# Performance work log

Measured on AMD Instinct MI355X. Metric: run time of the kernel, lower is better.

Reference implementation:

```python
import jax, jax.numpy as jnp
import numpy as np

EPS = 1e-12  # torch F.normalize eps
K = 32       # num_clusters (hardcoded in module)

def l2norm(v, axis):
    n = jnp.sqrt(jnp.sum(v * v, axis=axis, keepdims=True))
    return v / jnp.maximum(n, EPS)

def setup_inputs() -> dict:
    key = jax.random.key(0)
    k1, k2, k3, k4 = jax.random.split(key, 4)
    B, M, D = 64, 128, 2048
    x = jax.random.normal(k1, (B, M, D), dtype=jnp.float32)
    # ragged lengths in [1, M]
    lengths = jax.random.randint(k2, (B,), 0, M, dtype=jnp.int32) + 1
    init_sc = 1.0 / np.sqrt(D)
    W = init_sc * jax.random.normal(k3, (K, D), dtype=jnp.float32)  # fc1.weight
    C = init_sc * jax.random.normal(k4, (K, D), dtype=jnp.float32)  # centroids
    return {"x": x, "lengths": lengths, "W": W, "C": C}

def reference(x, lengths, W, C):
    # x: [B,M,D] padded frames, lengths: [B] valid frame counts
    B, M, D = x.shape
    mask = (jnp.arange(M)[None, :] < lengths[:, None]).astype(x.dtype)  # [B,M]
    cnt = lengths.astype(x.dtype)[:, None]                              # [B,1]
    # avg pooling over valid (raw, un-normalized) frames
    avgpool = jnp.sum(x * mask[:, :, None], axis=1) / cnt               # [B,D]
    # per-frame L2 normalize
    xn = l2norm(x, axis=-1)                                             # [B,M,D]
    # soft assignment: linear (no bias) + softmax over clusters
    logits = jnp.einsum('bmd,kd->bmk', xn, W)
    a = jax.nn.softmax(logits, axis=-1) * mask[:, :, None]              # [B,M,K]
    # VLAD residual aggregation, GEMM form:
    # sum_m a[b,m,k]*(xn[b,m,:] - C[k,:]) = (a^T xn) - C * sum_m a
    ax = jnp.einsum('bmk,bmd->bkd', a, xn)                              # [B,K,D]
    asum = jnp.sum(a, axis=1)                                           # [B,K]
    vlad = ax - asum[:, :, None] * C[None, :, :]                        # [B,K,D]
    # intra-normalize per cluster, flatten, global L2 normalize
    vlad = l2norm(vlad, axis=2)
    vlad = vlad.reshape(B, K * D)
    vlad = l2norm(vlad, axis=1)
    return jnp.concatenate([avgpool, vlad], axis=1)                     # [B, D + K*D]
```

## Files before the change

### kernel.cpp

```cpp
#include <hip/hip_runtime.h>
#include <math.h>

#define BB 64
#define MM 128
#define DDIM 2048
#define KK 32
#define NFR (BB*MM)
#define OUTROW (DDIM + KK*DDIM)

typedef __attribute__((ext_vector_type(8))) short bf16x8;
typedef __attribute__((ext_vector_type(4))) float f32x4;

__device__ __forceinline__ short f2bf(float f) {
  unsigned u = __builtin_bit_cast(unsigned, f);
  u += 0x7fffu + ((u >> 16) & 1u);
  return (short)(u >> 16);
}
__device__ __forceinline__ unsigned pack2(float lo, float hi) {
  return (unsigned)(unsigned short)f2bf(lo) | ((unsigned)(unsigned short)f2bf(hi) << 16);
}

__global__ __launch_bounds__(256) void k_prep(const float* __restrict__ W,
                                              short* __restrict__ Wb) {
  int i = (blockIdx.x * 256 + threadIdx.x) * 8;
  float4 a = *(const float4*)(W + i);
  float4 b = *(const float4*)(W + i + 4);
  bf16x8 o = {f2bf(a.x), f2bf(a.y), f2bf(a.z), f2bf(a.w),
              f2bf(b.x), f2bf(b.y), f2bf(b.z), f2bf(b.w)};
  *(bf16x8*)(Wb + i) = o;
}

__global__ __launch_bounds__(256, 2) void k_logits(const float* __restrict__ x,
    const int* __restrict__ lengths, const short* __restrict__ Wb,
    short* __restrict__ aT, float* __restrict__ asum_p) {
  const int t = threadIdx.x, wv = t >> 6, lane = t & 63;
  const int l15 = lane & 15, quad = lane >> 4;
  const int fg = blockIdx.x;
  const int g0 = fg * 16;
  const int b  = fg >> 3;
  const int m0 = (fg & 7) * 16;
  const int len = lengths[b];
  const bool av = (m0 + l15) < len;

  const float* xrow = x + (size_t)(g0 + l15) * DDIM + wv * 512 + quad * 8;
  const short* w0   = Wb + l15 * DDIM + wv * 512 + quad * 8;
  const short* w1   = w0 + 16 * DDIM;

  f32x4 c0 = {0.f, 0.f, 0.f, 0.f}, c1 = {0.f, 0.f, 0.f, 0.f};
  float ssq = 0.f;
  #pragma unroll
  for (int h = 0; h < 2; ++h) {
    float4 xa[8], xc[8];
    bf16x8 B0[8], B1[8];
    #pragma unroll
    for (int s = 0; s < 8; ++s) {
      const int so = h * 8 + s;
      if (av) {
        xa[s] = *(const float4*)(xrow + so * 32);
        xc[s] = *(const float4*)(xrow + so * 32 + 4);
      } else {
        xa[s] = make_float4(0.f, 0.f, 0.f, 0.f);
        xc[s] = make_float4(0.f, 0.f, 0.f, 0.f);
      }
      B0[s] = *(const bf16x8*)(w0 + so * 32);
      B1[s] = *(const bf16x8*)(w1 + so * 32);
    }
    #pragma unroll
    for (int s = 0; s < 8; ++s) {
      ssq = fmaf(xa[s].x, xa[s].x, ssq); ssq = fmaf(xa[s].y, xa[s].y, ssq);
      ssq = fmaf(xa[s].z, xa[s].z, ssq); ssq = fmaf(xa[s].w, xa[s].w, ssq);
      ssq = fmaf(xc[s].x, xc[s].x, ssq); ssq = fmaf(xc[s].y, xc[s].y, ssq);
      ssq = fmaf(xc[s].z, xc[s].z, ssq); ssq = fmaf(xc[s].w, xc[s].w, ssq);
      bf16x8 A = {f2bf(xa[s].x), f2bf(xa[s].y), f2bf(xa[s].z), f2bf(xa[s].w),
                  f2bf(xc[s].x), f2bf(xc[s].y), f2bf(xc[s].z), f2bf(xc[s].w)};
      c0 = __builtin_amdgcn_mfma_f32_16x16x32_bf16(A, B0[s], c0, 0, 0, 0);
      c1 = __builtin_amdgcn_mfma_f32_16x16x32_bf16(A, B1[s], c1, 0, 0, 0);
    }
  }

  ssq += __shfl_xor(ssq, 16, 64);
  ssq += __shfl_xor(ssq, 32, 64);
  __shared__ float sq[4][16];
  __shared__ float lg[4][16][33];
  if (quad == 0) sq[wv][l15] = ssq;
  #pragma unroll
  for (int r = 0; r < 4; ++r) {
    lg[wv][quad * 4 + r][l15]      = c0[r];
    lg[wv][quad * 4 + r][16 + l15] = c1[r];
  }
  __syncthreads();

  const int fr = t >> 4, kk = (t & 15) * 2;
  float s0 = 0.f, s1 = 0.f;
  #pragma unroll
  for (int w = 0; w < 4; ++w) { s0 += lg[w][fr][kk]; s1 += lg[w][fr][kk + 1]; }
  float ss  = sq[0][fr] + sq[1][fr] + sq[2][fr] + sq[3][fr];
  float inv = 1.f / fmaxf(sqrtf(ss), 1e-12f);
  s0 *= inv; s1 *= inv;
  float mx = fmaxf(s0, s1);
  mx = fmaxf(mx, __shfl_xor(mx, 1, 64));
  mx = fmaxf(mx, __shfl_xor(mx, 2, 64));
  mx = fmaxf(mx, __shfl_xor(mx, 4, 64));
  mx = fmaxf(mx, __shfl_xor(mx, 8, 64));
  float e0 = __expf(s0 - mx), e1 = __expf(s1 - mx);
  float se = e0 + e1;
  se += __shfl_xor(se, 1, 64);
  se += __shfl_xor(se, 2, 64);
  se += __shfl_xor(se, 4, 64);
  se += __shfl_xor(se, 8, 64);
  const bool valid = (m0 + fr) < len;
  float rr = valid ? (1.f / se) : 0.f;
  float a0 = e0 * rr, a1 = e1 * rr;

  __syncthreads();
  lg[0][fr][kk] = a0; lg[0][fr][kk + 1] = a1;
  __syncthreads();
  if (t < KK) {
    float s = 0.f;
    #pragma unroll
    for (int f = 0; f < 16; ++f) s += lg[0][f][t];
    asum_p[(size_t)fg * KK + t] = s;
  }
  short* ap = aT + (size_t)b * KK * MM + m0 + fr;
  ap[(size_t)kk * MM]       = f2bf(a0 * inv);
  ap[(size_t)(kk + 1) * MM] = f2bf(a1 * inv);
}

__global__ __launch_bounds__(256, 3) void k_vlad(const float* __restrict__ x,
    const int* __restrict__ lengths, const float* __restrict__ Cc,
    const short* __restrict__ aT, const float* __restrict__ asum_p,
    float* __restrict__ out, float* __restrict__ ssq_part) {
  const int t = threadIdx.x, wv = t >> 6, lane = t & 63;
  const int l15 = lane & 15, quad = lane >> 4;
  const int dc = blockIdx.x, b = blockIdx.y;
  const int dw0 = dc * 256 + wv * 64;
  const int len = lengths[b];

  __shared__ short xbt[4][64][40];
  __shared__ float vst[16][268];
  __shared__ float asl[KK];
  __shared__ float ss32[KK];

  if (t < KK) {
    float s = 0.f;
    #pragma unroll
    for (int p = 0; p < 8; ++p) s += asum_p[(size_t)(b * 8 + p) * KK + t];
    asl[t] = s;
  }

  const float* xb  = x  + (size_t)b * MM * DDIM;
  const short* at0 = aT + (size_t)b * KK * MM + (size_t)l15 * MM + quad * 8;

  const int q4   = l15 * 4;
  const int mrow = quad * 2;
  const int keyw = l15 & 3;
  const int keyr = (l15 >> 2) & 3;

  bf16x8 A0[4], A1[4];
  #pragma unroll
  for (int ms = 0; ms < 4; ++ms) {
    A0[ms] = *(const bf16x8*)(at0 + ms * 32);
    A1[ms] = *(const bf16x8*)(at0 + 16 * MM + ms * 32);
  }

  f32x4 acc[2][4];
  #pragma unroll
  for (int kt = 0; kt < 2; ++kt)
    #pragma unroll
    for (int nt = 0; nt < 4; ++nt) acc[kt][nt] = (f32x4){0.f, 0.f, 0.f, 0.f};
  float avg[4] = {0.f, 0.f, 0.f, 0.f};

  #pragma unroll
  for (int ms = 0; ms < 4; ++ms) {
    float4 v0[4], v1[4];
    #pragma unroll
    for (int p = 0; p < 4; ++p) {
      const int m = ms * 32 + p * 8 + mrow;
      const float* xr = xb + (size_t)m * DDIM + dw0 + q4;
      v0[p] = (m < len) ? *(const float4*)xr : make_float4(0.f, 0.f, 0.f, 0.f);
      v1[p] = (m + 1 < len) ? *(const float4*)(xr + DDIM)
                            : make_float4(0.f, 0.f, 0.f, 0.f);
    }
    #pragma unroll
    for (int p = 0; p < 4; ++p) {
      avg[0] += v0[p].x + v1[p].x;
      avg[1] += v0[p].y + v1[p].y;
      avg[2] += v0[p].z + v1[p].z;
      avg[3] += v0[p].w + v1[p].w;
      const int mls = (p ^ keyw) * 8 + mrow;
      *(unsigned*)&xbt[wv][q4 + 0][mls] = pack2(v0[p].x, v1[p].x);
      *(unsigned*)&xbt[wv][q4 + 1][mls] = pack2(v0[p].y, v1[p].y);
      *(unsigned*)&xbt[wv][q4 + 2][mls] = pack2(v0[p].z, v1[p].z);
      *(unsigned*)&xbt[wv][q4 + 3][mls] = pack2(v0[p].w, v1[p].w);
    }
    #pragma unroll
    for (int nt = 0; nt < 4; ++nt) {
      bf16x8 B = *(const bf16x8*)&xbt[wv][nt * 16 + l15][(quad ^ keyr) * 8];
      acc[0][nt] = __builtin_amdgcn_mfma_f32_16x16x32_bf16(A0[ms], B, acc[0][nt], 0, 0, 0);
      acc[1][nt] = __builtin_amdgcn_mfma_f32_16x16x32_bf16(A1[ms], B, acc[1][nt], 0, 0, 0);
    }
  }

  #pragma unroll
  for (int c = 0; c < 4; ++c) {
    avg[c] += __shfl_xor(avg[c], 16, 64);
    avg[c] += __shfl_xor(avg[c], 32, 64);
  }
  if (quad == 0) {
    float rl = 1.f / (float)len;
    *(float4*)(out + (size_t)b * OUTROW + dw0 + q4) =
        make_float4(avg[0] * rl, avg[1] * rl, avg[2] * rl, avg[3] * rl);
  }

  __syncthreads();
  float* orow = out + (size_t)b * OUTROW + DDIM;
  #pragma unroll
  for (int kt = 0; kt < 2; ++kt) {
    #pragma unroll
    for (int r = 0; r < 4; ++r) {
      const int kl = quad * 4 + r;
      const int k  = kt * 16 + kl;
      const float as = asl[k];
      #pragma unroll
      for (int nt = 0; nt < 4; ++nt) {
        const int d = dw0 + nt * 16 + l15;
        vst[kl][wv * 64 + nt * 16 + l15] =
            acc[kt][nt][r] - as * Cc[(size_t)k * DDIM + d];
      }
    }
    __syncthreads();
    #pragma unroll
    for (int it = 0; it < 4; ++it) {
      const int kl = it * 4 + wv;
      const int k  = kt * 16 + kl;
      float4 v = *(const float4*)&vst[kl][lane * 4];
      *(float4*)(orow + (size_t)k * DDIM + dc * 256 + lane * 4) = v;
      float sqv = fmaf(v.x, v.x, fmaf(v.y, v.y, fmaf(v.z, v.z, v.w * v.w)));
      sqv += __shfl_xor(sqv, 1, 64);
      sqv += __shfl_xor(sqv, 2, 64);
      sqv += __shfl_xor(sqv, 4, 64);
      sqv += __shfl_xor(sqv, 8, 64);
      sqv += __shfl_xor(sqv, 16, 64);
      sqv += __shfl_xor(sqv, 32, 64);
      if (lane == 0) ss32[k] = sqv;
    }
    __syncthreads();
  }
  if (t < KK)
    ssq_part[((size_t)dc * BB + b) * KK + t] = ss32[t];
}

__global__ __launch_bounds__(256) void k_norm(const float* __restrict__ ssq_part,
    float* __restrict__ out) {
  const int t = threadIdx.x;
  const int k = blockIdx.x;
  const int b = blockIdx.y;
  __shared__ float ssk[32];
  if (t < 32) {
    float sk = 0.f;
    #pragma unroll
    for (int dc = 0; dc < 8; ++dc)
      sk += ssq_part[((size_t)dc * BB + b) * KK + t];
    ssk[t] = sk;
  }
  __syncthreads();
  float gss = 0.f, iv_own = 0.f;
  #pragma unroll
  for (int kk = 0; kk < 32; ++kk) {
    float nk = sqrtf(ssk[kk]);
    float iv = 1.f / fmaxf(nk, 1e-12f);
    float nn = nk * iv;
    gss += nn * nn;
    if (kk == k) iv_own = iv;
  }
  float sc = iv_own / fmaxf(sqrtf(gss), 1e-12f);
  float* row = out + (size_t)b * OUTROW + DDIM + (size_t)k * DDIM;
  #pragma unroll
  for (int h = 0; h < 2; ++h) {
    float4* p = (float4*)(row + h * 1024 + t * 4);
    float4 v = *p;
    v.x *= sc; v.y *= sc; v.z *= sc; v.w *= sc;
    *p = v;
  }
}

extern "C" void kernel_launch(void* const* d_in, const int* in_sizes, int n_in,
                              void* d_out, int out_size, void* d_ws, size_t ws_size,
                              hipStream_t stream) {
  const float* x       = (const float*)d_in[0];
  const int*   lengths = (const int*)d_in[1];
  const float* W       = (const float*)d_in[2];
  const float* C       = (const float*)d_in[3];
  float* out = (float*)d_out;

  short* Wb     = (short*)d_ws;
  short* aT     = Wb + (size_t)KK * DDIM;
  float* asum_p = (float*)(aT + (size_t)BB * KK * MM);
  float* ssqp   = asum_p + (size_t)512 * KK;

  k_prep  <<<dim3(32),     256, 0, stream>>>(W, Wb);
  k_logits<<<dim3(512),    256, 0, stream>>>(x, lengths, Wb, aT, asum_p);
  k_vlad  <<<dim3(8, BB),  256, 0, stream>>>(x, lengths, C, aT, asum_p, out, ssqp);
  k_norm  <<<dim3(KK, BB), 256, 0, stream>>>(ssqp, out);
}
```

Before: 148.9 us.

## Split logits kernel into 8-frame blocks to double grid and raise occupancy

Each k_logits block now handles 8 frames instead of 16, doubling the grid to 1024 blocks. The stage loop is reorganised into smaller groups to cut register pressure, and launch bounds are raised to 4 blocks per SM. The softmax is rewritten so each thread owns one cluster, and the vlad kernel now sums 16 partials per batch. The MFMA tile is still 16 rows, so half of the A rows are zero padding and the W-fragment loads per frame double.

```diff
diff --git a/kernel.cpp b/kernel.cpp
--- a/kernel.cpp
+++ b/kernel.cpp
@@ -30,31 +30,31 @@
   *(bf16x8*)(Wb + i) = o;
 }
 
-__global__ __launch_bounds__(256, 2) void k_logits(const float* __restrict__ x,
+__global__ __launch_bounds__(256, 4) void k_logits(const float* __restrict__ x,
     const int* __restrict__ lengths, const short* __restrict__ Wb,
     short* __restrict__ aT, float* __restrict__ asum_p) {
   const int t = threadIdx.x, wv = t >> 6, lane = t & 63;
   const int l15 = lane & 15, quad = lane >> 4;
   const int fg = blockIdx.x;
-  const int g0 = fg * 16;
-  const int b  = fg >> 3;
-  const int m0 = (fg & 7) * 16;
+  const int g0 = fg * 8;
+  const int b  = fg >> 4;
+  const int m0 = (fg & 15) * 8;
   const int len = lengths[b];
-  const bool av = (m0 + l15) < len;
-
-  const float* xrow = x + (size_t)(g0 + l15) * DDIM + wv * 512 + quad * 8;
+  const bool av = (l15 < 8) && (m0 + l15 < len);
+
+  const float* xrow = x + (size_t)(g0 + (l15 & 7)) * DDIM + wv * 512 + quad * 8;
   const short* w0   = Wb + l15 * DDIM + wv * 512 + quad * 8;
   const short* w1   = w0 + 16 * DDIM;
 
   f32x4 c0 = {0.f, 0.f, 0.f, 0.f}, c1 = {0.f, 0.f, 0.f, 0.f};
-  float ssq = 0.f;
-  #pragma unroll
-  for (int h = 0; h < 2; ++h) {
-    float4 xa[8], xc[8];
-    bf16x8 B0[8], B1[8];
-    #pragma unroll
-    for (int s = 0; s < 8; ++s) {
-      const int so = h * 8 + s;
+  float sa = 0.f, sb = 0.f;
+  #pragma unroll
+  for (int g = 0; g < 4; ++g) {
+    float4 xa[4], xc[4];
+    bf16x8 B0[4], B1[4];
+    #pragma unroll
+    for (int s = 0; s < 4; ++s) {
+      const int so = g * 4 + s;
       if (av) {
         xa[s] = *(const float4*)(xrow + so * 32);
         xc[s] = *(const float4*)(xrow + so * 32 + 4);
@@ -66,11 +66,11 @@
       B1[s] = *(const bf16x8*)(w1 + so * 32);
     }
     #pragma unroll
-    for (int s = 0; s < 8; ++s) {
-      ssq = fmaf(xa[s].x, xa[s].x, ssq); ssq = fmaf(xa[s].y, xa[s].y, ssq);
-      ssq = fmaf(xa[s].z, xa[s].z, ssq); ssq = fmaf(xa[s].w, xa[s].w, ssq);
-      ssq = fmaf(xc[s].x, xc[s].x, ssq); ssq = fmaf(xc[s].y, xc[s].y, ssq);
-      ssq = fmaf(xc[s].z, xc[s].z, ssq); ssq = fmaf(xc[s].w, xc[s].w, ssq);
+    for (int s = 0; s < 4; ++s) {
+      sa = fmaf(xa[s].x, xa[s].x, sa); sb = fmaf(xa[s].y, xa[s].y, sb);
+      sa = fmaf(xa[s].z, xa[s].z, sa); sb = fmaf(xa[s].w, xa[s].w, sb);
+      sa = fmaf(xc[s].x, xc[s].x, sa); sb = fmaf(xc[s].y, xc[s].y, sb);
+      sa = fmaf(xc[s].z, xc[s].z, sa); sb = fmaf(xc[s].w, xc[s].w, sb);
       bf16x8 A = {f2bf(xa[s].x), f2bf(xa[s].y), f2bf(xa[s].z), f2bf(xa[s].w),
                   f2bf(xc[s].x), f2bf(xc[s].y), f2bf(xc[s].z), f2bf(xc[s].w)};
       c0 = __builtin_amdgcn_mfma_f32_16x16x32_bf16(A, B0[s], c0, 0, 0, 0);
@@ -78,52 +78,54 @@
     }
   }
 
+  float ssq = sa + sb;
   ssq += __shfl_xor(ssq, 16, 64);
   ssq += __shfl_xor(ssq, 32, 64);
-  __shared__ float sq[4][16];
-  __shared__ float lg[4][16][33];
-  if (quad == 0) sq[wv][l15] = ssq;
-  #pragma unroll
-  for (int r = 0; r < 4; ++r) {
-    lg[wv][quad * 4 + r][l15]      = c0[r];
-    lg[wv][quad * 4 + r][16 + l15] = c1[r];
-  }
-  __syncthreads();
-
-  const int fr = t >> 4, kk = (t & 15) * 2;
-  float s0 = 0.f, s1 = 0.f;
-  #pragma unroll
-  for (int w = 0; w < 4; ++w) { s0 += lg[w][fr][kk]; s1 += lg[w][fr][kk + 1]; }
-  float ss  = sq[0][fr] + sq[1][fr] + sq[2][fr] + sq[3][fr];
+  __shared__ float sq[4][8];
+  __shared__ float lg[4][8][33];
+  if (quad == 0 && l15 < 8) sq[wv][l15] = ssq;
+  if (quad < 2) {
+    #pragma unroll
+    for (int r = 0; r < 4; ++r) {
+      lg[wv][quad * 4 + r][l15]      = c0[r];
+      lg[wv][quad * 4 + r][16 + l15] = c1[r];
+    }
+  }
+  __syncthreads();
+
+  const int fr = t >> 5, kk = t & 31;
+  float s0 = 0.f;
+  #pragma unroll
+  for (int w = 0; w < 4; ++w) s0 += lg[w][fr][kk];
+  float ss = sq[0][fr] + sq[1][fr] + sq[2][fr] + sq[3][fr];
   float inv = 1.f / fmaxf(sqrtf(ss), 1e-12f);
-  s0 *= inv; s1 *= inv;
-  float mx = fmaxf(s0, s1);
+  s0 *= inv;
+  float mx = s0;
   mx = fmaxf(mx, __shfl_xor(mx, 1, 64));
   mx = fmaxf(mx, __shfl_xor(mx, 2, 64));
   mx = fmaxf(mx, __shfl_xor(mx, 4, 64));
   mx = fmaxf(mx, __shfl_xor(mx, 8, 64));
-  float e0 = __expf(s0 - mx), e1 = __expf(s1 - mx);
-  float se = e0 + e1;
+  mx = fmaxf(mx, __shfl_xor(mx, 16, 64));
+  float e0 = __expf(s0 - mx);
+  float se = e0;
   se += __shfl_xor(se, 1, 64);
   se += __shfl_xor(se, 2, 64);
   se += __shfl_xor(se, 4, 64);
   se += __shfl_xor(se, 8, 64);
+  se += __shfl_xor(se, 16, 64);
   const bool valid = (m0 + fr) < len;
-  float rr = valid ? (1.f / se) : 0.f;
-  float a0 = e0 * rr, a1 = e1 * rr;
-
-  __syncthreads();
-  lg[0][fr][kk] = a0; lg[0][fr][kk + 1] = a1;
+  float a0 = valid ? (e0 / se) : 0.f;
+
+  __syncthreads();
+  lg[0][fr][kk] = a0;
   __syncthreads();
   if (t < KK) {
     float s = 0.f;
     #pragma unroll
-    for (int f = 0; f < 16; ++f) s += lg[0][f][t];
+    for (int f = 0; f < 8; ++f) s += lg[0][f][t];
     asum_p[(size_t)fg * KK + t] = s;
   }
-  short* ap = aT + (size_t)b * KK * MM + m0 + fr;
-  ap[(size_t)kk * MM]       = f2bf(a0 * inv);
-  ap[(size_t)(kk + 1) * MM] = f2bf(a1 * inv);
+  aT[(size_t)b * KK * MM + (size_t)kk * MM + m0 + fr] = f2bf(a0 * inv);
 }
 
 __global__ __launch_bounds__(256, 3) void k_vlad(const float* __restrict__ x,
@@ -144,7 +146,7 @@
   if (t < KK) {
     float s = 0.f;
     #pragma unroll
-    for (int p = 0; p < 8; ++p) s += asum_p[(size_t)(b * 8 + p) * KK + t];
+    for (int p = 0; p < 16; ++p) s += asum_p[(size_t)(b * 16 + p) * KK + t];
     asl[t] = s;
   }
 
@@ -296,10 +298,10 @@
   short* Wb     = (short*)d_ws;
   short* aT     = Wb + (size_t)KK * DDIM;
   float* asum_p = (float*)(aT + (size_t)BB * KK * MM);
-  float* ssqp   = asum_p + (size_t)512 * KK;
+  float* ssqp   = asum_p + (size_t)1024 * KK;
 
   k_prep  <<<dim3(32),     256, 0, stream>>>(W, Wb);
-  k_logits<<<dim3(512),    256, 0, stream>>>(x, lengths, Wb, aT, asum_p);
+  k_logits<<<dim3(1024),   256, 0, stream>>>(x, lengths, Wb, aT, asum_p);
   k_vlad  <<<dim3(8, BB),  256, 0, stream>>>(x, lengths, C, aT, asum_p, out, ssqp);
   k_norm  <<<dim3(KK, BB), 256, 0, stream>>>(ssqp, out);
 }
```

Result: slower. 183.9 us (+23.5%).
